# Kernel optimization log

Hardware: AMD Instinct MI355X
Metric: run time of the kernel (lower is better)

The kernel has to match this reference:

```python
import jax, jax.numpy as jnp
import numpy as np

N = 1024      # number of residues/tokens
D = 768       # node feature dim (heads * d_head)
H = 12        # heads
DH = D // H   # d_head = 64
DP = 128      # pair feature dim
SCALE = 0.125 # 1/sqrt(d_head)
EPS = 1e-5

def _ln(x, w, b):
    m = jnp.mean(x, axis=-1, keepdims=True)
    v = jnp.var(x, axis=-1, keepdims=True)
    return (x - m) * jax.lax.rsqrt(v + EPS) * w + b

def setup_inputs() -> dict:
    key = jax.random.key(0)
    ks = jax.random.split(key, 8)
    s = 0.02
    return {
        "node_feats": jax.random.normal(ks[0], (N, D), dtype=jnp.float32),
        "pair_feats": jax.random.normal(ks[1], (N, N, DP), dtype=jnp.float32),
        "ln_node_w": jnp.ones((D,), jnp.float32), "ln_node_b": jnp.zeros((D,), jnp.float32),
        "pair_ln_w": jnp.ones((DP,), jnp.float32), "pair_ln_b": jnp.zeros((DP,), jnp.float32),
        "qkv_W": jax.random.normal(ks[2], (D, 3 * D), dtype=jnp.float32) * s,
        "qkv_b": jnp.zeros((3 * D,), jnp.float32),
        "q_ln_w": jnp.ones((D,), jnp.float32), "q_ln_b": jnp.zeros((D,), jnp.float32),
        "k_ln_w": jnp.ones((D,), jnp.float32), "k_ln_b": jnp.zeros((D,), jnp.float32),
        "g_W": jax.random.normal(ks[3], (D, D), dtype=jnp.float32) * s,
        "g_b": jnp.zeros((D,), jnp.float32),
        "bias_W": jax.random.normal(ks[4], (DP, H), dtype=jnp.float32) * s,
        "bias_b": jnp.zeros((H,), jnp.float32),
        "out_W": jax.random.normal(ks[5], (D, D), dtype=jnp.float32) * s,
        "out_b": jnp.zeros((D,), jnp.float32),
        "mask": jax.random.bernoulli(ks[6], 0.9, (N, N)),
    }

def reference(node_feats, pair_feats, ln_node_w, ln_node_b, pair_ln_w, pair_ln_b,
              qkv_W, qkv_b, q_ln_w, q_ln_b, k_ln_w, k_ln_b,
              g_W, g_b, bias_W, bias_b, out_W, out_b, mask):
    x = _ln(node_feats, ln_node_w, ln_node_b)                 # [N, D]
    p = _ln(pair_feats, pair_ln_w, pair_ln_b)                 # [N, N, DP]
    q, k, v = jnp.split(x @ qkv_W + qkv_b, 3, axis=-1)        # each [N, D]
    q = _ln(q, q_ln_w, q_ln_b)
    k = _ln(k, k_ln_w, k_ln_b)
    g = x @ g_W + g_b                                         # [N, D]
    bias = jnp.einsum('ijp,ph->hij', p, bias_W) + bias_b[:, None, None]  # [H, N, N]
    bias = bias + jnp.where(mask[None, :, :], 0.0, -10000.0)
    q = q.reshape(N, H, DH); k = k.reshape(N, H, DH); v = v.reshape(N, H, DH)
    logits = jnp.einsum('ihd,jhd->hij', q, k) * SCALE + bias  # [H, N, N]
    attn = jax.nn.softmax(logits, axis=-1)
    out = jnp.einsum('hij,jhd->ihd', attn, v).reshape(N, D)   # [N, D]
    out = jax.nn.sigmoid(g) * out
    return out @ out_W + out_b
```

## Files before the change

### kernel.cpp

```cpp
#include <hip/hip_runtime.h>
#include <math.h>

#define N_TOK 1024
#define D_DIM 768
#define H_N   12
#define DH    64
#define DP    128
#define SCALE 0.125f
#define EPS   1e-5f
#define NN    (N_TOK * N_TOK)

__global__ __launch_bounds__(128) void prep_kernel(
    const float* __restrict__ pair_ln_w, const float* __restrict__ pair_ln_b,
    const float* __restrict__ bias_W, const float* __restrict__ bias_b,
    float* __restrict__ W2, float* __restrict__ S2cb)
{
    __shared__ float Ws[DP * H_N];
    __shared__ float slw[DP], slb[DP];
    int t = threadIdx.x;
    slw[t] = pair_ln_w[t];
    slb[t] = pair_ln_b[t];
    for (int idx = t; idx < DP * H_N; idx += 128) Ws[idx] = bias_W[idx];
    __syncthreads();
    for (int idx = t; idx < DP * H_N; idx += 128) {
        int c = idx / H_N;
        W2[idx] = slw[c] * Ws[idx];
    }
    if (t < 24) {
        int h = t % H_N;
        bool isS = t < H_N;
        float s = 0.f;
        for (int c = 0; c < DP; ++c)
            s += (isS ? slw[c] : slb[c]) * Ws[c * H_N + h];
        S2cb[t] = isS ? s : (s + bias_b[h]);
    }
}

__global__ __launch_bounds__(256) void ln_kernel(
    const float* __restrict__ in, float* __restrict__ out,
    int istride, int ostride,
    const float* __restrict__ w, const float* __restrict__ b)
{
    int row = blockIdx.x;
    int tid = threadIdx.x;
    const float* ip = in + (size_t)row * istride;
    float v0 = ip[tid], v1 = ip[tid + 256], v2 = ip[tid + 512];
    float s = v0 + v1 + v2;
    float q = v0 * v0 + v1 * v1 + v2 * v2;
    __shared__ float red[8];
    #pragma unroll
    for (int o = 32; o > 0; o >>= 1) {
        s += __shfl_down(s, o);
        q += __shfl_down(q, o);
    }
    int lane = tid & 63, wv = tid >> 6;
    if (lane == 0) { red[wv] = s; red[4 + wv] = q; }
    __syncthreads();
    if (tid == 0) {
        float ss = red[0] + red[1] + red[2] + red[3];
        float qq = red[4] + red[5] + red[6] + red[7];
        float mean = ss * (1.f / 768.f);
        float var = qq * (1.f / 768.f) - mean * mean;
        red[0] = mean;
        red[1] = rsqrtf(var + EPS);
    }
    __syncthreads();
    float mean = red[0], rstd = red[1];
    float* op = out + (size_t)row * ostride;
    op[tid]       = (v0 - mean) * rstd * w[tid]       + b[tid];
    op[tid + 256] = (v1 - mean) * rstd * w[tid + 256] + b[tid + 256];
    op[tid + 512] = (v2 - mean) * rstd * w[tid + 512] + b[tid + 512];
}

__global__ __launch_bounds__(256) void sgemm(
    const float* __restrict__ A, int lda,
    const float* __restrict__ B0, int ldb0, const float* __restrict__ bias0,
    const float* __restrict__ B1, int ldb1, const float* __restrict__ bias1,
    int split, float* __restrict__ C, int ldc, int K)
{
    __shared__ float As[16 * 68];
    __shared__ float Bs[16 * 68];
    int tid = threadIdx.x;
    int tx = tid & 15, ty = tid >> 4;
    int m0 = blockIdx.y * 64, n0 = blockIdx.x * 64;
    const float* Bp; const float* bp; int ldb, bcol0;
    if (n0 < split) { Bp = B0; bp = bias0; ldb = ldb0; bcol0 = n0; }
    else            { Bp = B1; bp = bias1; ldb = ldb1; bcol0 = n0 - split; }

    float acc[4][4] = {};
    int ar = tid >> 2, ak = (tid & 3) * 4;
    int bk = tid >> 4, bc = (tid & 15) * 4;

    for (int kt = 0; kt < K; kt += 16) {
        float4 av = *(const float4*)&A[(size_t)(m0 + ar) * lda + kt + ak];
        float4 bv = *(const float4*)&Bp[(size_t)(kt + bk) * ldb + bcol0 + bc];
        As[(ak + 0) * 68 + ar] = av.x;
        As[(ak + 1) * 68 + ar] = av.y;
        As[(ak + 2) * 68 + ar] = av.z;
        As[(ak + 3) * 68 + ar] = av.w;
        *(float4*)&Bs[bk * 68 + bc] = bv;
        __syncthreads();
        #pragma unroll
        for (int kk = 0; kk < 16; ++kk) {
            float4 a = *(const float4*)&As[kk * 68 + ty * 4];
            float4 b = *(const float4*)&Bs[kk * 68 + tx * 4];
            acc[0][0] += a.x * b.x; acc[0][1] += a.x * b.y; acc[0][2] += a.x * b.z; acc[0][3] += a.x * b.w;
            acc[1][0] += a.y * b.x; acc[1][1] += a.y * b.y; acc[1][2] += a.y * b.z; acc[1][3] += a.y * b.w;
            acc[2][0] += a.z * b.x; acc[2][1] += a.z * b.y; acc[2][2] += a.z * b.z; acc[2][3] += a.z * b.w;
            acc[3][0] += a.w * b.x; acc[3][1] += a.w * b.y; acc[3][2] += a.w * b.z; acc[3][3] += a.w * b.w;
        }
        __syncthreads();
    }
    float4 bb = *(const float4*)&bp[bcol0 + tx * 4];
    #pragma unroll
    for (int u = 0; u < 4; ++u) {
        float4 o;
        o.x = acc[u][0] + bb.x; o.y = acc[u][1] + bb.y;
        o.z = acc[u][2] + bb.z; o.w = acc[u][3] + bb.w;
        *(float4*)&C[(size_t)(m0 + ty * 4 + u) * ldc + n0 + tx * 4] = o;
    }
}

__global__ __launch_bounds__(256) void bias_kernel(
    const float* __restrict__ pair, const int* __restrict__ mask,
    const float* __restrict__ W2, const float* __restrict__ S2cb,
    float* __restrict__ biasbuf)
{
    __shared__ float sW2[DP * H_N];
    __shared__ float sS[H_N], sC[H_N];
    int tid = threadIdx.x;
    for (int t = tid; t < DP * H_N; t += 256) sW2[t] = W2[t];
    if (tid < H_N) { sS[tid] = S2cb[tid]; sC[tid] = S2cb[H_N + tid]; }
    __syncthreads();

    int gid = blockIdx.x * 256 + tid;
    const float4* p4 = (const float4*)(pair + (size_t)gid * DP);
    float sum = 0.f, ssq = 0.f;
    float dot[H_N];
    #pragma unroll
    for (int h = 0; h < H_N; ++h) dot[h] = 0.f;

    #pragma unroll 4
    for (int c4 = 0; c4 < 32; ++c4) {
        float4 v = p4[c4];
        float e[4] = { v.x, v.y, v.z, v.w };
        #pragma unroll
        for (int k = 0; k < 4; ++k) {
            float x = e[k];
            sum += x; ssq += x * x;
            const float* wp = &sW2[(c4 * 4 + k) * H_N];
            #pragma unroll
            for (int h = 0; h < H_N; ++h) dot[h] += x * wp[h];
        }
    }
    float mean = sum * (1.f / 128.f);
    float var  = ssq * (1.f / 128.f) - mean * mean;
    float rstd = rsqrtf(var + EPS);
    float mz = (mask[gid] != 0) ? 0.f : -10000.f;
    #pragma unroll
    for (int h = 0; h < H_N; ++h)
        biasbuf[(size_t)h * NN + gid] = (dot[h] - mean * sS[h]) * rstd + sC[h] + mz;
}

__global__ __launch_bounds__(256) void attn_kernel(
    const float* __restrict__ xw, const float* __restrict__ biasbuf,
    float* __restrict__ attn_out)
{
    const int h  = blockIdx.y;
    const int i0 = blockIdx.x * 16;
    const int tid = threadIdx.x;
    const int tx = tid & 15, ty = tid >> 4;

    __shared__ float Qs[16 * 65];
    __shared__ float Ks[32 * 65];
    __shared__ float Vs[32 * 68];
    __shared__ float Ps[16 * 33];

    {
        int r = tid >> 4, c4 = (tid & 15) * 4;
        float4 v = *(const float4*)(xw + (size_t)(i0 + r) * 3072 + h * 64 + c4);
        float* d = &Qs[r * 65 + c4];
        d[0] = v.x * SCALE; d[1] = v.y * SCALE; d[2] = v.z * SCALE; d[3] = v.w * SCALE;
    }

    float m = -1e30f, l = 0.f;
    float a0 = 0.f, a1 = 0.f, a2 = 0.f, a3 = 0.f;
    const float* brow = biasbuf + (size_t)h * NN + (size_t)(i0 + ty) * N_TOK;

    for (int j0 = 0; j0 < N_TOK; j0 += 32) {
        #pragma unroll
        for (int q2 = 0; q2 < 2; ++q2) {
            int idx = tid + q2 * 256;
            int r = idx >> 4, c4 = (idx & 15) * 4;
            const float* kb = xw + (size_t)(j0 + r) * 3072 + 768 + h * 64 + c4;
            float4 kv = *(const float4*)kb;
            float* kd = &Ks[r * 65 + c4];
            kd[0] = kv.x; kd[1] = kv.y; kd[2] = kv.z; kd[3] = kv.w;
            float4 vv = *(const float4*)(kb + 768);
            *(float4*)&Vs[r * 68 + c4] = vv;
        }
        __syncthreads();

        float s0 = 0.f, s1 = 0.f;
        const float* qrow = &Qs[ty * 65];
        const float* k0 = &Ks[(2 * tx) * 65];
        const float* k1 = k0 + 65;
        #pragma unroll
        for (int d = 0; d < 64; ++d) {
            float qv = qrow[d];
            s0 += qv * k0[d];
            s1 += qv * k1[d];
        }
        s0 += brow[j0 + 2 * tx];
        s1 += brow[j0 + 2 * tx + 1];

        float mt = fmaxf(s0, s1);
        #pragma unroll
        for (int o = 1; o < 16; o <<= 1) mt = fmaxf(mt, __shfl_xor(mt, o));
        float mn = fmaxf(m, mt);
        float al = __expf(m - mn);
        float p0 = __expf(s0 - mn);
        float p1 = __expf(s1 - mn);
        float rs = p0 + p1;
        #pragma unroll
        for (int o = 1; o < 16; o <<= 1) rs += __shfl_xor(rs, o);
        l = l * al + rs;
        m = mn;
        a0 *= al; a1 *= al; a2 *= al; a3 *= al;
        Ps[ty * 33 + 2 * tx]     = p0;
        Ps[ty * 33 + 2 * tx + 1] = p1;
        __syncthreads();

        const float* prow = &Ps[ty * 33];
        #pragma unroll
        for (int j = 0; j < 32; ++j) {
            float pv = prow[j];
            float4 vv = *(const float4*)&Vs[j * 68 + tx * 4];
            a0 += pv * vv.x; a1 += pv * vv.y; a2 += pv * vv.z; a3 += pv * vv.w;
        }
        __syncthreads();
    }

    float inv = 1.f / l;
    int row = i0 + ty;
    float4 gv = *(const float4*)(xw + (size_t)row * 3072 + 2304 + h * 64 + tx * 4);
    float* op = attn_out + (size_t)row * 768 + h * 64 + tx * 4;
    op[0] = a0 * inv / (1.f + __expf(-gv.x));
    op[1] = a1 * inv / (1.f + __expf(-gv.y));
    op[2] = a2 * inv / (1.f + __expf(-gv.z));
    op[3] = a3 * inv / (1.f + __expf(-gv.w));
}

extern "C" void kernel_launch(void* const* d_in, const int* in_sizes, int n_in,
                              void* d_out, int out_size, void* d_ws, size_t ws_size,
                              hipStream_t stream)
{
    const float* node      = (const float*)d_in[0];
    const float* pair      = (const float*)d_in[1];
    const float* ln_node_w = (const float*)d_in[2];
    const float* ln_node_b = (const float*)d_in[3];
    const float* pair_ln_w = (const float*)d_in[4];
    const float* pair_ln_b = (const float*)d_in[5];
    const float* qkv_W     = (const float*)d_in[6];
    const float* qkv_b     = (const float*)d_in[7];
    const float* q_ln_w    = (const float*)d_in[8];
    const float* q_ln_b    = (const float*)d_in[9];
    const float* k_ln_w    = (const float*)d_in[10];
    const float* k_ln_b    = (const float*)d_in[11];
    const float* g_W       = (const float*)d_in[12];
    const float* g_b       = (const float*)d_in[13];
    const float* bias_W    = (const float*)d_in[14];
    const float* bias_b    = (const float*)d_in[15];
    const float* out_W     = (const float*)d_in[16];
    const float* out_b     = (const float*)d_in[17];
    const int*   mask      = (const int*)d_in[18];
    float* out = (float*)d_out;

    float* ws      = (float*)d_ws;
    float* x       = ws;
    float* xw      = x + 786432;
    float* W2      = xw + 3145728;
    float* S2cb    = W2 + 1536;
    float* biasbuf = S2cb + 32;
    float* attn_o  = biasbuf + 12582912;

    prep_kernel<<<1, 128, 0, stream>>>(pair_ln_w, pair_ln_b, bias_W, bias_b, W2, S2cb);
    ln_kernel<<<1024, 256, 0, stream>>>(node, x, 768, 768, ln_node_w, ln_node_b);
    sgemm<<<dim3(48, 16), 256, 0, stream>>>(x, 768,
                                            qkv_W, 2304, qkv_b,
                                            g_W, 768, g_b,
                                            2304, xw, 3072, 768);
    ln_kernel<<<1024, 256, 0, stream>>>(xw, xw, 3072, 3072, q_ln_w, q_ln_b);
    ln_kernel<<<1024, 256, 0, stream>>>(xw + 768, xw + 768, 3072, 3072, k_ln_w, k_ln_b);
    bias_kernel<<<4096, 256, 0, stream>>>(pair, mask, W2, S2cb, biasbuf);
    attn_kernel<<<dim3(64, 12), 256, 0, stream>>>(xw, biasbuf, attn_o);
    sgemm<<<dim3(12, 16), 256, 0, stream>>>(attn_o, 768,
                                            out_W, 768, out_b,
                                            out_W, 768, out_b,
                                            1 << 30, out, 768, 768);
}
```

Before: 1.089 ms.

## Process four pair positions per thread in bias kernel and vectorize attention dot products

The bias kernel now has each thread handle four pair positions. The weights are transposed to a head-major float4 layout, so every shared-memory weight read is reused across four positions, and the grid shrinks from 4096 to 1024 blocks. In the attention kernel the Q and K tiles use a 72-float row stride, which lets the QK dot product use float4 loads from shared memory. These changes cut LDS traffic and instruction count in the bias and logit computations, at the cost of higher register pressure and possible bank conflicts from the new padding.

```diff
diff --git a/kernel.cpp b/kernel.cpp
--- a/kernel.cpp
+++ b/kernel.cpp
@@ -13,7 +13,7 @@
 __global__ __launch_bounds__(128) void prep_kernel(
     const float* __restrict__ pair_ln_w, const float* __restrict__ pair_ln_b,
     const float* __restrict__ bias_W, const float* __restrict__ bias_b,
-    float* __restrict__ W2, float* __restrict__ S2cb)
+    float* __restrict__ W2T, float* __restrict__ S2cb)
 {
     __shared__ float Ws[DP * H_N];
     __shared__ float slw[DP], slb[DP];
@@ -23,8 +23,8 @@
     for (int idx = t; idx < DP * H_N; idx += 128) Ws[idx] = bias_W[idx];
     __syncthreads();
     for (int idx = t; idx < DP * H_N; idx += 128) {
-        int c = idx / H_N;
-        W2[idx] = slw[c] * Ws[idx];
+        int h = idx / DP, c = idx % DP;
+        W2T[idx] = slw[c] * Ws[c * H_N + h];
     }
     if (t < 24) {
         int h = t % H_N;
@@ -121,45 +121,64 @@
     }
 }
 
+#define BP 4
 __global__ __launch_bounds__(256) void bias_kernel(
     const float* __restrict__ pair, const int* __restrict__ mask,
-    const float* __restrict__ W2, const float* __restrict__ S2cb,
+    const float* __restrict__ W2T, const float* __restrict__ S2cb,
     float* __restrict__ biasbuf)
 {
-    __shared__ float sW2[DP * H_N];
+    __shared__ float4 sW4[H_N * 32];
     __shared__ float sS[H_N], sC[H_N];
     int tid = threadIdx.x;
-    for (int t = tid; t < DP * H_N; t += 256) sW2[t] = W2[t];
+    for (int t = tid; t < H_N * 32; t += 256)
+        sW4[t] = ((const float4*)W2T)[t];
     if (tid < H_N) { sS[tid] = S2cb[tid]; sC[tid] = S2cb[H_N + tid]; }
     __syncthreads();
 
-    int gid = blockIdx.x * 256 + tid;
-    const float4* p4 = (const float4*)(pair + (size_t)gid * DP);
-    float sum = 0.f, ssq = 0.f;
-    float dot[H_N];
-    #pragma unroll
-    for (int h = 0; h < H_N; ++h) dot[h] = 0.f;
-
-    #pragma unroll 4
+    int base = blockIdx.x * (256 * BP) + tid;
+    const float4* p4 = (const float4*)(pair + (size_t)base * DP);
+
+    float dot[H_N][BP];
+    #pragma unroll
+    for (int h = 0; h < H_N; ++h)
+        #pragma unroll
+        for (int p = 0; p < BP; ++p) dot[h][p] = 0.f;
+    float sum[BP], ssq[BP];
+    #pragma unroll
+    for (int p = 0; p < BP; ++p) { sum[p] = 0.f; ssq[p] = 0.f; }
+
     for (int c4 = 0; c4 < 32; ++c4) {
-        float4 v = p4[c4];
-        float e[4] = { v.x, v.y, v.z, v.w };
-        #pragma unroll
-        for (int k = 0; k < 4; ++k) {
-            float x = e[k];
-            sum += x; ssq += x * x;
-            const float* wp = &sW2[(c4 * 4 + k) * H_N];
+        float4 pv[BP];
+        #pragma unroll
+        for (int p = 0; p < BP; ++p)
+            pv[p] = p4[(size_t)p * (256 * DP / 4) + c4];
+        #pragma unroll
+        for (int p = 0; p < BP; ++p) {
+            sum[p] += pv[p].x + pv[p].y + pv[p].z + pv[p].w;
+            ssq[p] += pv[p].x * pv[p].x + pv[p].y * pv[p].y
+                    + pv[p].z * pv[p].z + pv[p].w * pv[p].w;
+        }
+        #pragma unroll
+        for (int h = 0; h < H_N; ++h) {
+            float4 w = sW4[h * 32 + c4];
             #pragma unroll
-            for (int h = 0; h < H_N; ++h) dot[h] += x * wp[h];
-        }
-    }
-    float mean = sum * (1.f / 128.f);
-    float var  = ssq * (1.f / 128.f) - mean * mean;
-    float rstd = rsqrtf(var + EPS);
-    float mz = (mask[gid] != 0) ? 0.f : -10000.f;
-    #pragma unroll
-    for (int h = 0; h < H_N; ++h)
-        biasbuf[(size_t)h * NN + gid] = (dot[h] - mean * sS[h]) * rstd + sC[h] + mz;
+            for (int p = 0; p < BP; ++p)
+                dot[h][p] += pv[p].x * w.x + pv[p].y * w.y
+                           + pv[p].z * w.z + pv[p].w * w.w;
+        }
+    }
+
+    #pragma unroll
+    for (int p = 0; p < BP; ++p) {
+        int pos = base + p * 256;
+        float mean = sum[p] * (1.f / 128.f);
+        float var  = ssq[p] * (1.f / 128.f) - mean * mean;
+        float rstd = rsqrtf(var + EPS);
+        float mz = (mask[pos] != 0) ? 0.f : -10000.f;
+        #pragma unroll
+        for (int h = 0; h < H_N; ++h)
+            biasbuf[(size_t)h * NN + pos] = (dot[h][p] - mean * sS[h]) * rstd + sC[h] + mz;
+    }
 }
 
 __global__ __launch_bounds__(256) void attn_kernel(
@@ -171,15 +190,15 @@
     const int tid = threadIdx.x;
     const int tx = tid & 15, ty = tid >> 4;
 
-    __shared__ float Qs[16 * 65];
-    __shared__ float Ks[32 * 65];
+    __shared__ float Qs[16 * 72];
+    __shared__ float Ks[32 * 72];
     __shared__ float Vs[32 * 68];
     __shared__ float Ps[16 * 33];
 
     {
         int r = tid >> 4, c4 = (tid & 15) * 4;
         float4 v = *(const float4*)(xw + (size_t)(i0 + r) * 3072 + h * 64 + c4);
-        float* d = &Qs[r * 65 + c4];
+        float* d = &Qs[r * 72 + c4];
         d[0] = v.x * SCALE; d[1] = v.y * SCALE; d[2] = v.z * SCALE; d[3] = v.w * SCALE;
     }
 
@@ -194,22 +213,21 @@
             int r = idx >> 4, c4 = (idx & 15) * 4;
             const float* kb = xw + (size_t)(j0 + r) * 3072 + 768 + h * 64 + c4;
             float4 kv = *(const float4*)kb;
-            float* kd = &Ks[r * 65 + c4];
-            kd[0] = kv.x; kd[1] = kv.y; kd[2] = kv.z; kd[3] = kv.w;
+            *(float4*)&Ks[r * 72 + c4] = kv;
             float4 vv = *(const float4*)(kb + 768);
             *(float4*)&Vs[r * 68 + c4] = vv;
         }
         __syncthreads();
 
         float s0 = 0.f, s1 = 0.f;
-        const float* qrow = &Qs[ty * 65];
-        const float* k0 = &Ks[(2 * tx) * 65];
-        const float* k1 = k0 + 65;
-        #pragma unroll
-        for (int d = 0; d < 64; ++d) {
-            float qv = qrow[d];
-            s0 += qv * k0[d];
-            s1 += qv * k1[d];
+        const float4* q4 = (const float4*)&Qs[ty * 72];
+        const float4* k0 = (const float4*)&Ks[(2 * tx) * 72];
+        const float4* k1 = (const float4*)&Ks[(2 * tx + 1) * 72];
+        #pragma unroll
+        for (int d4 = 0; d4 < 16; ++d4) {
+            float4 qv = q4[d4], ka = k0[d4], kb2 = k1[d4];
+            s0 += qv.x * ka.x  + qv.y * ka.y  + qv.z * ka.z  + qv.w * ka.w;
+            s1 += qv.x * kb2.x + qv.y * kb2.y + qv.z * kb2.z + qv.w * kb2.w;
         }
         s0 += brow[j0 + 2 * tx];
         s1 += brow[j0 + 2 * tx + 1];
@@ -279,12 +297,12 @@
     float* ws      = (float*)d_ws;
     float* x       = ws;
     float* xw      = x + 786432;
-    float* W2      = xw + 3145728;
-    float* S2cb    = W2 + 1536;
+    float* W2T     = xw + 3145728;
+    float* S2cb    = W2T + 1536;
     float* biasbuf = S2cb + 32;
     float* attn_o  = biasbuf + 12582912;
 
-    prep_kernel<<<1, 128, 0, stream>>>(pair_ln_w, pair_ln_b, bias_W, bias_b, W2, S2cb);
+    prep_kernel<<<1, 128, 0, stream>>>(pair_ln_w, pair_ln_b, bias_W, bias_b, W2T, S2cb);
     ln_kernel<<<1024, 256, 0, stream>>>(node, x, 768, 768, ln_node_w, ln_node_b);
     sgemm<<<dim3(48, 16), 256, 0, stream>>>(x, 768,
                                             qkv_W, 2304, qkv_b,
@@ -292,7 +310,7 @@
                                             2304, xw, 3072, 768);
     ln_kernel<<<1024, 256, 0, stream>>>(xw, xw, 3072, 3072, q_ln_w, q_ln_b);
     ln_kernel<<<1024, 256, 0, stream>>>(xw + 768, xw + 768, 3072, 3072, k_ln_w, k_ln_b);
-    bias_kernel<<<4096, 256, 0, stream>>>(pair, mask, W2, S2cb, biasbuf);
+    bias_kernel<<<1024, 256, 0, stream>>>(pair, mask, W2T, S2cb, biasbuf);
     attn_kernel<<<dim3(64, 12), 256, 0, stream>>>(xw, biasbuf, attn_o);
     sgemm<<<dim3(12, 16), 256, 0, stream>>>(attn_o, 768,
                                             out_W, 768, out_b,
```

After: 1.490 ms. 1.37x slower.
